# Kernel tuning notes

Hardware: AMD Instinct MI355X
Metric: run time of the kernel (lower is better)

## Reference

```python
import jax, jax.numpy as jnp
import numpy as np
import math

B, C, N, M = 4, 128, 4096, 4096

def setup_inputs() -> dict:
    key = jax.random.key(0)
    ks = jax.random.split(key, 8)
    return {
        "x1": jax.random.normal(ks[0], (B, C, N), dtype=jnp.float32),
        "p1": jax.random.normal(ks[1], (B, 3, N), dtype=jnp.float32),
        "x2": jax.random.normal(ks[2], (B, C, M), dtype=jnp.float32),
        "p2": jax.random.normal(ks[3], (B, 3, M), dtype=jnp.float32),
        "Wq": jax.random.normal(ks[4], (C, C), dtype=jnp.float32) * 0.05,
        "Wk": jax.random.normal(ks[5], (C, C), dtype=jnp.float32) * 0.05,
        "Wv": jax.random.normal(ks[6], (C, C), dtype=jnp.float32) * 0.05,
        "Wpos": jax.random.normal(ks[7], (C, 3), dtype=jnp.float32) * 0.05,
    }

def reference(x1, p1, x2, p2, Wq, Wk, Wv, Wpos):
    # Conv1d with kernel_size=1, no bias == per-point matmul over channel dim.
    # NOTE: original forward uses self.pos for BOTH p1 and p2 (pos1 conv unused).
    pos = jnp.einsum('ck,bkn->bcn', Wpos, p1)   # [B,C,N]
    pos1 = jnp.einsum('ck,bkm->bcm', Wpos, p2)  # [B,C,M]
    q = jnp.einsum('dc,bcn->bdn', Wq, x1 + pos)   # [B,C,N]
    k = jnp.einsum('dc,bcm->bdm', Wk, x2 + pos1)  # [B,C,M]
    v = jnp.einsum('dc,bcm->bdm', Wv, x2)         # [B,C,M]
    scale = math.sqrt(q.shape[1])  # sqrt(C) -- q.shape[-2] in (B,C,N) layout
    energy = jnp.einsum('bcn,bcm->bnm', q, k) / scale  # [B,N,M]
    attention = jax.nn.softmax(energy, axis=-1)
    vout = jnp.einsum('bnm,bcm->bnc', attention, v)    # [B,N,C]
    out = jnp.swapaxes(vout, 1, 2) + x1                # [B,C,N] residual
    return jnp.swapaxes(out, 1, 2)                     # [B,N,C]
```

## Files before the change

### kernel.cpp

```cpp
#include <hip/hip_runtime.h>
#include <hip/hip_bf16.h>

#define B_ 4
#define C_ 128
#define N_ 4096
#define M_ 4096

typedef __bf16 bf16;
typedef __bf16 bf16x8 __attribute__((ext_vector_type(8)));
typedef float f32x4 __attribute__((ext_vector_type(4)));
typedef float f32x16 __attribute__((ext_vector_type(16)));
typedef unsigned u32x2 __attribute__((ext_vector_type(2)));

#define MFMA16(a, b, c) __builtin_amdgcn_mfma_f32_16x16x32_bf16(a, b, c, 0, 0, 0)
#define MFMA32(a, b, c) __builtin_amdgcn_mfma_f32_32x32x16_bf16(a, b, c, 0, 0, 0)

__device__ inline void gll16(const bf16* g, bf16* l) {
    __builtin_amdgcn_global_load_lds(
        (const __attribute__((address_space(1))) void*)g,
        (__attribute__((address_space(3))) void*)l, 16, 0, 0);
}

__device__ inline unsigned cvtpk(float a, float b) {
    unsigned r;
    asm("v_cvt_pk_bf16_f32 %0, %1, %2" : "=v"(r) : "v"(a), "v"(b));
    return r;
}

__global__ __launch_bounds__(256) void wcvt_kernel(
    const float* __restrict__ Wq, const float* __restrict__ Wk,
    const float* __restrict__ Wv, bf16* __restrict__ Wb) {
    int i = (blockIdx.x * 256 + threadIdx.x) * 4;
    const float* src = (i < 16384) ? Wq : (i < 32768) ? Wk : Wv;
    float scale = (i < 16384) ? 0.12752107168406815f : 1.0f;
    int off = i & 16383;
    float4 v = *(const float4*)(src + off);
    union { ushort4 u4; bf16 h[4]; } pk;
    pk.h[0] = (bf16)(v.x * scale); pk.h[1] = (bf16)(v.y * scale);
    pk.h[2] = (bf16)(v.z * scale); pk.h[3] = (bf16)(v.w * scale);
    *(ushort4*)(Wb + i) = pk.u4;
}

__global__ __launch_bounds__(256) void kvproj_kernel(
    const float* __restrict__ x2, const float* __restrict__ p2,
    const bf16* __restrict__ Wb, const float* __restrict__ Wpos,
    bf16* __restrict__ Kt, bf16* __restrict__ Vt) {
    __shared__ __align__(16) bf16 xp2[32 * 136];
    __shared__ __align__(16) bf16 xr2[32 * 136];
    __shared__ float pp[3 * 32], wls[384];

    const int t = threadIdx.x;
    const int b = blockIdx.y;
    const int n0 = blockIdx.x * 32;

    if (t < 24) {
        int k3 = t / 8, i4 = (t & 7) * 4;
        *(float4*)&pp[k3 * 32 + i4] =
            *(const float4*)(p2 + ((size_t)b * 3 + k3) * N_ + n0 + i4);
    } else if (t < 120) {
        int i4 = (t - 24) * 4;
        *(float4*)&wls[i4] = *(const float4*)(Wpos + i4);
    }
    __syncthreads();

    #pragma unroll
    for (int k = 0; k < 4; ++k) {
        int s = t + k * 256;
        int c = s >> 3, n4 = (s & 7) * 4;
        float4 xv = *(const float4*)(x2 + ((size_t)b * C_ + c) * N_ + n0 + n4);
        float w0 = wls[c * 3 + 0], w1 = wls[c * 3 + 1], w2 = wls[c * 3 + 2];
        const float* xa = &xv.x;
        #pragma unroll
        for (int j = 0; j < 4; ++j) {
            float pos = w0 * pp[n4 + j] + w1 * pp[32 + n4 + j] + w2 * pp[64 + n4 + j];
            xp2[(n4 + j) * 136 + c] = (bf16)(xa[j] + pos);
            xr2[(n4 + j) * 136 + c] = (bf16)xa[j];
        }
    }
    __syncthreads();

    const int w = t >> 6;
    const int lane = t & 63;
    const int col = lane & 15, quad = lane >> 4;
    const int band = w & 1;
    const int nl = band * 16 + col;
    const bool isK = (w < 2);

    const bf16* src = isK ? xp2 : xr2;
    const bf16* Wm = Wb + (isK ? 16384 : 32768);

    bf16x8 bx[4];
    #pragma unroll
    for (int cs = 0; cs < 4; ++cs)
        bx[cs] = *(const bf16x8*)&src[nl * 136 + cs * 32 + quad * 8];

    if (isK) {
        #pragma unroll
        for (int dt = 0; dt < 8; ++dt) {
            f32x4 acc = {0.f, 0.f, 0.f, 0.f};
            #pragma unroll
            for (int cs = 0; cs < 4; ++cs) {
                bf16x8 wf = *(const bf16x8*)(Wm + (dt * 16 + col) * 128 + cs * 32 + quad * 8);
                acc = MFMA16(bx[cs], wf, acc);
            }
            #pragma unroll
            for (int r = 0; r < 4; ++r) {
                int n = n0 + band * 16 + quad * 4 + r;
                Kt[((size_t)b * N_ + n) * C_ + dt * 16 + col] = (bf16)acc[r];
            }
        }
    } else {
        #pragma unroll
        for (int dt = 0; dt < 8; ++dt) {
            f32x4 acc = {0.f, 0.f, 0.f, 0.f};
            #pragma unroll
            for (int cs = 0; cs < 4; ++cs) {
                bf16x8 wf = *(const bf16x8*)(Wm + (dt * 16 + col) * 128 + cs * 32 + quad * 8);
                acc = MFMA16(wf, bx[cs], acc);
            }
            #pragma unroll
            for (int r = 0; r < 4; ++r)
                Vt[((size_t)b * C_ + dt * 16 + quad * 4 + r) * (size_t)M_ + n0 + nl] = (bf16)acc[r];
        }
    }
}

__global__ __launch_bounds__(512) void attn_kernel(
    const bf16* __restrict__ Kt, const bf16* __restrict__ Vt,
    const float* __restrict__ x1, const float* __restrict__ p1,
    const bf16* __restrict__ Wb, const float* __restrict__ Wpos,
    float* __restrict__ out) {
    __shared__ __align__(16) char smem[132096];

    const int t = threadIdx.x;
    const int w = t >> 6;
    const int lane = t & 63;
    const int col = lane & 31;
    const int hi = lane >> 5;
    const int kg = w & 3;
    const int qg = w >> 2;

    const int g0 = blockIdx.x;
    const int xcd = g0 & 7;
    const int b = xcd >> 1;
    const int qt = (xcd & 1) + ((g0 >> 3) << 1);
    const int n0 = qt * 64;

    const bf16* Kbase = Kt + (size_t)b * M_ * C_;
    const bf16* Vbase = Vt + (size_t)b * C_ * M_;

    bf16* xq = (bf16*)smem;
    float* ppq = (float*)(smem + 17408);
    float* wlsq = (float*)(smem + 18176);

    if (t < 48) {
        int k3 = t / 16, i4 = (t & 15) * 4;
        *(float4*)&ppq[k3 * 64 + i4] =
            *(const float4*)(p1 + ((size_t)b * 3 + k3) * N_ + n0 + i4);
    } else if (t < 144) {
        int i4 = (t - 48) * 4;
        *(float4*)&wlsq[i4] = *(const float4*)(Wpos + i4);
    }
    __syncthreads();

    #pragma unroll
    for (int k = 0; k < 4; ++k) {
        int s = t + k * 512;
        int c = s >> 4, n4 = (s & 15) * 4;
        float4 xv = *(const float4*)(x1 + ((size_t)b * C_ + c) * N_ + n0 + n4);
        float w0 = wlsq[c * 3 + 0], w1 = wlsq[c * 3 + 1], w2 = wlsq[c * 3 + 2];
        const float* xa = &xv.x;
        #pragma unroll
        for (int j = 0; j < 4; ++j) {
            float pos = w0 * ppq[n4 + j] + w1 * ppq[64 + n4 + j] + w2 * ppq[128 + n4 + j];
            xq[(n4 + j) * 136 + c] = (bf16)(xa[j] + pos);
        }
    }
    __syncthreads();

    {
        const int colq = lane & 15, quadq = lane >> 4;
        const int nlq = (w & 3) * 16 + colq;
        bf16x8 bxq[4];
        #pragma unroll
        for (int cs = 0; cs < 4; ++cs)
            bxq[cs] = *(const bf16x8*)&xq[nlq * 136 + cs * 32 + quadq * 8];
        __syncthreads();
        const int dt0 = (w >> 2) * 4;
        #pragma unroll
        for (int di = 0; di < 4; ++di) {
            int dt = dt0 + di;
            f32x4 acc = {0.f, 0.f, 0.f, 0.f};
            #pragma unroll
            for (int cs = 0; cs < 4; ++cs) {
                bf16x8 wf = *(const bf16x8*)(Wb + (dt * 16 + colq) * 128 + cs * 32 + quadq * 8);
                acc = MFMA16(bxq[cs], wf, acc);
            }
            #pragma unroll
            for (int r = 0; r < 4; ++r)
                xq[((w & 3) * 16 + quadq * 4 + r) * 136 + dt * 16 + colq] = (bf16)acc[r];
        }
        __syncthreads();
    }

    bf16x8 qf[8];
    #pragma unroll
    for (int cs = 0; cs < 8; ++cs)
        qf[cs] = *(const bf16x8*)&xq[(qg * 32 + col) * 136 + cs * 16 + hi * 8];
    asm volatile("s_waitcnt lgkmcnt(0)" ::: "memory");
    __builtin_amdgcn_sched_barrier(0);
    __builtin_amdgcn_s_barrier();

    f32x16 oacc[4];
    #pragma unroll
    for (int i = 0; i < 4; ++i)
        #pragma unroll
        for (int j = 0; j < 16; ++j) oacc[i][j] = 0.f;
    f32x16 Z;
    #pragma unroll
    for (int j = 0; j < 16; ++j) Z[j] = 0.f;
    float lacc = 0.f;

    const int key_l = (kg << 5) + col;
    const int kxor = (key_l & 15) << 4;

    int kaddr[8];
    #pragma unroll
    for (int cs = 0; cs < 8; ++cs)
        kaddr[cs] = key_l * 256 + (((((cs << 1) + hi)) << 4) ^ kxor);
    const int vaddrA = 65536 + col * 256 + (((((kg << 2) + hi)) << 4) ^ ((col & 15) << 4));
    const int vaddrB = vaddrA ^ 32;

    const bf16* Kchunk = Kbase;
    const bf16* Vchunk = Vbase;
    int koff[4], voff[4];
    #pragma unroll
    for (int i = 0; i < 4; ++i) {
        int g = ((w << 2) + i) * 64 + lane;
        int row = g >> 4;
        int sp = (g & 15) ^ (row & 15);
        koff[i] = row * C_ + sp * 8;
        voff[i] = row * M_ + sp * 8;
    }

    auto stage = [&](int kbDst, int vbDst) {
        #pragma unroll
        for (int i = 0; i < 4; ++i)
            gll16(Kchunk + koff[i], (bf16*)(smem + kbDst) + ((w << 2) + i) * 512);
        #pragma unroll
        for (int i = 0; i < 4; ++i)
            gll16(Vchunk + voff[i], (bf16*)(smem + vbDst) + ((w << 2) + i) * 512);
        Kchunk += 128 * C_;
        Vchunk += 128;
    };

    auto body = [&](int kbImm, int vbImm, int kbDst, int vbDst, bool doStage) {
        asm volatile("s_waitcnt vmcnt(0)" ::: "memory");
        __builtin_amdgcn_sched_barrier(0);
        __builtin_amdgcn_s_barrier();
        __builtin_amdgcn_sched_barrier(0);
        if (doStage) stage(kbDst, vbDst);

        __builtin_amdgcn_s_setprio(1);
        bf16x8 kf0 = *(const bf16x8*)(smem + kbImm + kaddr[0]);
        f32x16 sacc = MFMA32(kf0, qf[0], Z);
        #pragma unroll
        for (int cs = 1; cs < 8; ++cs) {
            bf16x8 kf = *(const bf16x8*)(smem + kbImm + kaddr[cs]);
            sacc = MFMA32(kf, qf[cs], sacc);
        }
        __builtin_amdgcn_s_setprio(0);

        float p[16];
        #pragma unroll
        for (int r = 0; r < 16; ++r)
            p[r] = __builtin_amdgcn_exp2f(sacc[r]);
        {
            float s01 = (p[0] + p[1]) + (p[2] + p[3]);
            float s23 = (p[4] + p[5]) + (p[6] + p[7]);
            float s45 = (p[8] + p[9]) + (p[10] + p[11]);
            float s67 = (p[12] + p[13]) + (p[14] + p[15]);
            lacc += (s01 + s23) + (s45 + s67);
        }
        unsigned W0 = cvtpk(p[0], p[1]),  W1 = cvtpk(p[2], p[3]);
        unsigned W2 = cvtpk(p[4], p[5]),  W3 = cvtpk(p[6], p[7]);
        unsigned W4 = cvtpk(p[8], p[9]),  W5 = cvtpk(p[10], p[11]);
        unsigned W6 = cvtpk(p[12], p[13]), W7 = cvtpk(p[14], p[15]);
        uint4 u0, u1;
#if __has_builtin(__builtin_amdgcn_permlane32_swap)
        u32x2 r0 = __builtin_amdgcn_permlane32_swap(W0, W2, false, false);
        u0.x = r0[0]; u0.z = r0[1];
        u32x2 r1 = __builtin_amdgcn_permlane32_swap(W1, W3, false, false);
        u0.y = r1[0]; u0.w = r1[1];
        u32x2 r2 = __builtin_amdgcn_permlane32_swap(W4, W6, false, false);
        u1.x = r2[0]; u1.z = r2[1];
        u32x2 r3 = __builtin_amdgcn_permlane32_swap(W5, W7, false, false);
        u1.y = r3[0]; u1.w = r3[1];
#else
        unsigned X0 = hi ? W0 : W2, X1 = hi ? W1 : W3;
        unsigned Y0 = hi ? W4 : W6, Y1 = hi ? W5 : W7;
        X0 = __shfl_xor(X0, 32, 64);  X1 = __shfl_xor(X1, 32, 64);
        Y0 = __shfl_xor(Y0, 32, 64);  Y1 = __shfl_xor(Y1, 32, 64);
        u0.x = hi ? X0 : W0;  u0.y = hi ? X1 : W1;
        u0.z = hi ? W2 : X0;  u0.w = hi ? W3 : X1;
        u1.x = hi ? Y0 : W4;  u1.y = hi ? Y1 : W5;
        u1.z = hi ? W6 : Y0;  u1.w = hi ? W7 : Y1;
#endif
        bf16x8 af0 = __builtin_bit_cast(bf16x8, u0);
        bf16x8 af1 = __builtin_bit_cast(bf16x8, u1);

        __builtin_amdgcn_s_setprio(1);
        #pragma unroll
        for (int ct = 0; ct < 4; ++ct) {
            bf16x8 vf0 = *(const bf16x8*)(smem + vbImm + ct * 8192 + vaddrA);
            bf16x8 vf1 = *(const bf16x8*)(smem + vbImm + ct * 8192 + vaddrB);
            oacc[ct] = MFMA32(af0, vf0, oacc[ct]);
            oacc[ct] = MFMA32(af1, vf1, oacc[ct]);
        }
        __builtin_amdgcn_s_setprio(0);

        asm volatile("s_waitcnt lgkmcnt(0)" ::: "memory");
        __builtin_amdgcn_sched_barrier(0);
    };

    stage(0, 65536);
    #pragma unroll 1
    for (int jp = 0; jp < 16; ++jp) {
        body(0, 0, 32768, 98304, true);
        body(32768, 32768, 0, 65536, jp < 15);
    }

    __builtin_amdgcn_s_barrier();

    float* obuf = (float*)smem;
    float* lps  = (float*)(smem + 131072);

    lacc += __shfl_xor(lacc, 32, 64);
    if (hi == 0) lps[(kg << 6) + (qg << 5) + col] = lacc;

    #pragma unroll
    for (int ct = 0; ct < 4; ++ct)
        #pragma unroll
        for (int r = 0; r < 16; ++r) {
            int q = (r & 3) + ((r >> 2) << 3) + (hi << 2);
            obuf[kg * 8192 + ((qg << 5) + q) * 128 + (ct << 5) + col] = oacc[ct][r];
        }
    __syncthreads();

    const int c2 = lane << 1;
    #pragma unroll
    for (int j = 0; j < 8; ++j) {
        int q = (w << 3) + j;
        float s0 = 0.f, s1 = 0.f;
        #pragma unroll
        for (int pp2_ = 0; pp2_ < 4; ++pp2_) {
            float2 v = *(const float2*)&obuf[pp2_ * 8192 + q * 128 + c2];
            s0 += v.x; s1 += v.y;
        }
        float lsum = lps[q] + lps[64 + q] + lps[128 + q] + lps[192 + q];
        float linv = 1.0f / lsum;
        int n = n0 + q;
        float o0 = s0 * linv + x1[((size_t)b * C_ + c2) * N_ + n];
        float o1 = s1 * linv + x1[((size_t)b * C_ + c2 + 1) * N_ + n];
        *(float2*)&out[((size_t)b * N_ + n) * C_ + c2] = make_float2(o0, o1);
    }
}

extern "C" void kernel_launch(void* const* d_in, const int* in_sizes, int n_in,
                              void* d_out, int out_size, void* d_ws, size_t ws_size,
                              hipStream_t stream) {
    const float* x1   = (const float*)d_in[0];
    const float* p1   = (const float*)d_in[1];
    const float* x2   = (const float*)d_in[2];
    const float* p2   = (const float*)d_in[3];
    const float* Wq   = (const float*)d_in[4];
    const float* Wk   = (const float*)d_in[5];
    const float* Wv   = (const float*)d_in[6];
    const float* Wpos = (const float*)d_in[7];
    float* out = (float*)d_out;

    bf16* Wb = (bf16*)d_ws;
    bf16* Kt = Wb + 65536;
    bf16* Vt = Kt + (size_t)B_ * N_ * C_;

    wcvt_kernel<<<dim3(48), dim3(256), 0, stream>>>(Wq, Wk, Wv, Wb);
    kvproj_kernel<<<dim3(128, B_), dim3(256), 0, stream>>>(
        x2, p2, Wb, Wpos, Kt, Vt);
    attn_kernel<<<dim3(256), dim3(512), 0, stream>>>(
        Kt, Vt, x1, p1, Wb, Wpos, out);
}
```

Measured before the change: 137.2 us.

## Halve query tile per block, split keys across eight waves, stage K/V separately

Each block now handles 32 queries instead of 64 and the grid doubles to 512 blocks. All eight waves split the keys of a 256-key chunk, replacing the 4x2 query/key wave grid. The K/V double buffer is replaced by single buffers for K and V, each reloaded as soon as its previous contents are consumed, with a finer vmcnt wait pattern. The intent is more blocks to fill the CUs and less per-block serialization, at the cost of reading K/V twice as often overall, an 8-way reduction at the end, and less load/compute overlap.

Result: slower. 149.2 us (+8.7%).

```diff
diff --git a/kernel.cpp b/kernel.cpp
--- a/kernel.cpp
+++ b/kernel.cpp
@@ -137,42 +137,40 @@
     const int lane = t & 63;
     const int col = lane & 31;
     const int hi = lane >> 5;
-    const int kg = w & 3;
-    const int qg = w >> 2;
 
     const int g0 = blockIdx.x;
     const int xcd = g0 & 7;
     const int b = xcd >> 1;
     const int qt = (xcd & 1) + ((g0 >> 3) << 1);
-    const int n0 = qt * 64;
+    const int n0 = qt * 32;
 
     const bf16* Kbase = Kt + (size_t)b * M_ * C_;
     const bf16* Vbase = Vt + (size_t)b * C_ * M_;
 
     bf16* xq = (bf16*)smem;
-    float* ppq = (float*)(smem + 17408);
-    float* wlsq = (float*)(smem + 18176);
-
-    if (t < 48) {
-        int k3 = t / 16, i4 = (t & 15) * 4;
-        *(float4*)&ppq[k3 * 64 + i4] =
+    float* ppq = (float*)(smem + 8704);
+    float* wlsq = (float*)(smem + 9216);
+
+    if (t < 24) {
+        int k3 = t / 8, i4 = (t & 7) * 4;
+        *(float4*)&ppq[k3 * 32 + i4] =
             *(const float4*)(p1 + ((size_t)b * 3 + k3) * N_ + n0 + i4);
-    } else if (t < 144) {
-        int i4 = (t - 48) * 4;
+    } else if (t < 120) {
+        int i4 = (t - 24) * 4;
         *(float4*)&wlsq[i4] = *(const float4*)(Wpos + i4);
     }
     __syncthreads();
 
     #pragma unroll
-    for (int k = 0; k < 4; ++k) {
+    for (int k = 0; k < 2; ++k) {
         int s = t + k * 512;
-        int c = s >> 4, n4 = (s & 15) * 4;
+        int c = s >> 3, n4 = (s & 7) * 4;
         float4 xv = *(const float4*)(x1 + ((size_t)b * C_ + c) * N_ + n0 + n4);
         float w0 = wlsq[c * 3 + 0], w1 = wlsq[c * 3 + 1], w2 = wlsq[c * 3 + 2];
         const float* xa = &xv.x;
         #pragma unroll
         for (int j = 0; j < 4; ++j) {
-            float pos = w0 * ppq[n4 + j] + w1 * ppq[64 + n4 + j] + w2 * ppq[128 + n4 + j];
+            float pos = w0 * ppq[n4 + j] + w1 * ppq[32 + n4 + j] + w2 * ppq[64 + n4 + j];
             xq[(n4 + j) * 136 + c] = (bf16)(xa[j] + pos);
         }
     }
@@ -180,15 +178,15 @@
 
     {
         const int colq = lane & 15, quadq = lane >> 4;
-        const int nlq = (w & 3) * 16 + colq;
+        const int nlq = (w & 1) * 16 + colq;
         bf16x8 bxq[4];
         #pragma unroll
         for (int cs = 0; cs < 4; ++cs)
             bxq[cs] = *(const bf16x8*)&xq[nlq * 136 + cs * 32 + quadq * 8];
         __syncthreads();
-        const int dt0 = (w >> 2) * 4;
-        #pragma unroll
-        for (int di = 0; di < 4; ++di) {
+        const int dt0 = (w >> 1) * 2;
+        #pragma unroll
+        for (int di = 0; di < 2; ++di) {
             int dt = dt0 + di;
             f32x4 acc = {0.f, 0.f, 0.f, 0.f};
             #pragma unroll
@@ -198,7 +196,7 @@
             }
             #pragma unroll
             for (int r = 0; r < 4; ++r)
-                xq[((w & 3) * 16 + quadq * 4 + r) * 136 + dt * 16 + colq] = (bf16)acc[r];
+                xq[((w & 1) * 16 + quadq * 4 + r) * 136 + dt * 16 + colq] = (bf16)acc[r];
         }
         __syncthreads();
     }
@@ -206,7 +204,7 @@
     bf16x8 qf[8];
     #pragma unroll
     for (int cs = 0; cs < 8; ++cs)
-        qf[cs] = *(const bf16x8*)&xq[(qg * 32 + col) * 136 + cs * 16 + hi * 8];
+        qf[cs] = *(const bf16x8*)&xq[col * 136 + cs * 16 + hi * 8];
     asm volatile("s_waitcnt lgkmcnt(0)" ::: "memory");
     __builtin_amdgcn_sched_barrier(0);
     __builtin_amdgcn_s_barrier();
@@ -221,55 +219,62 @@
     for (int j = 0; j < 16; ++j) Z[j] = 0.f;
     float lacc = 0.f;
 
-    const int key_l = (kg << 5) + col;
+    const int key_l = (w << 5) + col;
     const int kxor = (key_l & 15) << 4;
 
     int kaddr[8];
     #pragma unroll
     for (int cs = 0; cs < 8; ++cs)
         kaddr[cs] = key_l * 256 + (((((cs << 1) + hi)) << 4) ^ kxor);
-    const int vaddrA = 65536 + col * 256 + (((((kg << 2) + hi)) << 4) ^ ((col & 15) << 4));
+    const int vaddrA = 65536 + col * 512 + ((((w << 2) + hi) ^ col) << 4);
     const int vaddrB = vaddrA ^ 32;
 
     const bf16* Kchunk = Kbase;
     const bf16* Vchunk = Vbase;
-    int koff[4], voff[4];
-    #pragma unroll
-    for (int i = 0; i < 4; ++i) {
-        int g = ((w << 2) + i) * 64 + lane;
-        int row = g >> 4;
-        int sp = (g & 15) ^ (row & 15);
-        koff[i] = row * C_ + sp * 8;
-        voff[i] = row * M_ + sp * 8;
-    }
-
-    auto stage = [&](int kbDst, int vbDst) {
-        #pragma unroll
-        for (int i = 0; i < 4; ++i)
-            gll16(Kchunk + koff[i], (bf16*)(smem + kbDst) + ((w << 2) + i) * 512);
-        #pragma unroll
-        for (int i = 0; i < 4; ++i)
-            gll16(Vchunk + voff[i], (bf16*)(smem + vbDst) + ((w << 2) + i) * 512);
-        Kchunk += 128 * C_;
-        Vchunk += 128;
+    int koff[8], voff[8];
+    #pragma unroll
+    for (int i = 0; i < 8; ++i) {
+        int g = (w << 9) + (i << 6) + lane;
+        int krow = g >> 4;
+        koff[i] = krow * C_ + ((g & 15) ^ (krow & 15)) * 8;
+        int vrow = g >> 5;
+        voff[i] = vrow * M_ + ((g & 31) ^ (vrow & 31)) * 8;
+    }
+
+    auto stageK = [&]() {
+        #pragma unroll
+        for (int i = 0; i < 8; ++i)
+            gll16(Kchunk + koff[i], (bf16*)smem + (w << 12) + (i << 9) + lane * 8);
+        Kchunk += 256 * C_;
     };
-
-    auto body = [&](int kbImm, int vbImm, int kbDst, int vbDst, bool doStage) {
-        asm volatile("s_waitcnt vmcnt(0)" ::: "memory");
+    auto stageV = [&]() {
+        #pragma unroll
+        for (int i = 0; i < 8; ++i)
+            gll16(Vchunk + voff[i], (bf16*)(smem + 65536) + (w << 12) + (i << 9) + lane * 8);
+        Vchunk += 256;
+    };
+
+    stageK();
+    stageV();
+
+    #pragma unroll 1
+    for (int ch = 0; ch < 16; ++ch) {
+        asm volatile("s_waitcnt vmcnt(8)" ::: "memory");
         __builtin_amdgcn_sched_barrier(0);
-        __builtin_amdgcn_s_barrier();
+
+        __builtin_amdgcn_s_setprio(1);
+        bf16x8 kf0 = *(const bf16x8*)(smem + kaddr[0]);
+        f32x16 sacc = MFMA32(kf0, qf[0], Z);
+        #pragma unroll
+        for (int cs = 1; cs < 8; ++cs) {
+            bf16x8 kf = *(const bf16x8*)(smem + kaddr[cs]);
+            sacc = MFMA32(kf, qf[cs], sacc);
+        }
+        __builtin_amdgcn_s_setprio(0);
+
+        asm volatile("s_waitcnt lgkmcnt(0)" ::: "memory");
         __builtin_amdgcn_sched_barrier(0);
-        if (doStage) stage(kbDst, vbDst);
-
-        __builtin_amdgcn_s_setprio(1);
-        bf16x8 kf0 = *(const bf16x8*)(smem + kbImm + kaddr[0]);
-        f32x16 sacc = MFMA32(kf0, qf[0], Z);
-        #pragma unroll
-        for (int cs = 1; cs < 8; ++cs) {
-            bf16x8 kf = *(const bf16x8*)(smem + kbImm + kaddr[cs]);
-            sacc = MFMA32(kf, qf[cs], sacc);
-        }
-        __builtin_amdgcn_s_setprio(0);
+        if (ch < 15) stageK();
 
         float p[16];
         #pragma unroll
@@ -309,11 +314,16 @@
         bf16x8 af0 = __builtin_bit_cast(bf16x8, u0);
         bf16x8 af1 = __builtin_bit_cast(bf16x8, u1);
 
+        if (ch < 15) asm volatile("s_waitcnt vmcnt(8)" ::: "memory");
+        else         asm volatile("s_waitcnt vmcnt(0)" ::: "memory");
+        __builtin_amdgcn_sched_barrier(0);
+        __builtin_amdgcn_s_barrier();
+
         __builtin_amdgcn_s_setprio(1);
         #pragma unroll
         for (int ct = 0; ct < 4; ++ct) {
-            bf16x8 vf0 = *(const bf16x8*)(smem + vbImm + ct * 8192 + vaddrA);
-            bf16x8 vf1 = *(const bf16x8*)(smem + vbImm + ct * 8192 + vaddrB);
+            bf16x8 vf0 = *(const bf16x8*)(smem + ct * 16384 + vaddrA);
+            bf16x8 vf1 = *(const bf16x8*)(smem + ct * 16384 + vaddrB);
             oacc[ct] = MFMA32(af0, vf0, oacc[ct]);
             oacc[ct] = MFMA32(af1, vf1, oacc[ct]);
         }
@@ -321,13 +331,8 @@
 
         asm volatile("s_waitcnt lgkmcnt(0)" ::: "memory");
         __builtin_amdgcn_sched_barrier(0);
-    };
-
-    stage(0, 65536);
-    #pragma unroll 1
-    for (int jp = 0; jp < 16; ++jp) {
-        body(0, 0, 32768, 98304, true);
-        body(32768, 32768, 0, 65536, jp < 15);
+        __builtin_amdgcn_s_barrier();
+        if (ch < 15) stageV();
     }
 
     __builtin_amdgcn_s_barrier();
@@ -336,28 +341,29 @@
     float* lps  = (float*)(smem + 131072);
 
     lacc += __shfl_xor(lacc, 32, 64);
-    if (hi == 0) lps[(kg << 6) + (qg << 5) + col] = lacc;
+    if (hi == 0) lps[(w << 5) + col] = lacc;
 
     #pragma unroll
     for (int ct = 0; ct < 4; ++ct)
         #pragma unroll
         for (int r = 0; r < 16; ++r) {
             int q = (r & 3) + ((r >> 2) << 3) + (hi << 2);
-            obuf[kg * 8192 + ((qg << 5) + q) * 128 + (ct << 5) + col] = oacc[ct][r];
+            obuf[w * 4096 + q * 128 + (ct << 5) + col] = oacc[ct][r];
         }
     __syncthreads();
 
     const int c2 = lane << 1;
     #pragma unroll
-    for (int j = 0; j < 8; ++j) {
-        int q = (w << 3) + j;
+    for (int j = 0; j < 4; ++j) {
+        int q = (w << 2) + j;
         float s0 = 0.f, s1 = 0.f;
-        #pragma unroll
-        for (int pp2_ = 0; pp2_ < 4; ++pp2_) {
-            float2 v = *(const float2*)&obuf[pp2_ * 8192 + q * 128 + c2];
+        float lsum = 0.f;
+        #pragma unroll
+        for (int p8 = 0; p8 < 8; ++p8) {
+            float2 v = *(const float2*)&obuf[p8 * 4096 + q * 128 + c2];
             s0 += v.x; s1 += v.y;
-        }
-        float lsum = lps[q] + lps[64 + q] + lps[128 + q] + lps[192 + q];
+            lsum += lps[p8 * 32 + q];
+        }
         float linv = 1.0f / lsum;
         int n = n0 + q;
         float o0 = s0 * linv + x1[((size_t)b * C_ + c2) * N_ + n];
@@ -386,6 +392,6 @@
     wcvt_kernel<<<dim3(48), dim3(256), 0, stream>>>(Wq, Wk, Wv, Wb);
     kvproj_kernel<<<dim3(128, B_), dim3(256), 0, stream>>>(
         x2, p2, Wb, Wpos, Kt, Vt);
-    attn_kernel<<<dim3(256), dim3(512), 0, stream>>>(
+    attn_kernel<<<dim3(512), dim3(512), 0, stream>>>(
         Kt, Vt, x1, p1, Wb, Wpos, out);
 }
```
